# Performance work log

Measured on AMD Instinct MI355X. Metric: run time of the kernel, lower is better.

## Reference

```python
import jax, jax.numpy as jnp
import numpy as np

IN_F = 4096
OUT_F = 16384
TOKENS = 64


def setup_inputs() -> dict:
    key = jax.random.key(0)
    k1, k2, k3 = jax.random.split(key, 3)
    x = jax.random.normal(k1, (TOKENS, IN_F), dtype=jnp.float16)
    # int8-valued weights stored as int32 (same math after cast to fp16)
    weight = jax.random.randint(k2, (OUT_F, IN_F), -127, 127, dtype=jnp.int32)
    weight_scales = jax.random.uniform(k3, (OUT_F,), dtype=jnp.float16, minval=0.001, maxval=0.02)
    bias = jnp.zeros((1, OUT_F), dtype=jnp.float16)
    return {"x": x, "weight": weight, "weight_scales": weight_scales, "bias": bias}


def reference(x, weight, weight_scales, bias):
    # Dequantize int8 weight to fp16 with per-output-channel scale, then linear.
    w_fp16 = weight.astype(jnp.float16) * weight_scales[:, None]  # [out, in]
    y = jnp.dot(x, w_fp16.T) + bias  # [tokens, out]
    return y
```

## Files before the change

### kernel.cpp

```cpp
#include <hip/hip_runtime.h>
#include <hip/hip_bf16.h>
#include <hip/hip_fp16.h>

#define IN_F 4096
#define OUT_F 16384
#define TOKENS 64

#define NT 32
#define KT 128
#define KHALF 2048
#define NTILES 16
#define TILE_BYTES (NT * KT * 4)
#define BLOCK 256

typedef __attribute__((ext_vector_type(8))) short bf16x8;
typedef __attribute__((ext_vector_type(8))) unsigned short u16x8;
typedef __attribute__((ext_vector_type(4))) float f32x4;
typedef __attribute__((ext_vector_type(4))) int i32x4;

enum { F_BF16 = 0, F_FP16 = 1, F_FP32 = 2 };

__device__ __forceinline__ float dec_bf16(unsigned short h) {
    return __uint_as_float(((unsigned)h) << 16);
}
__device__ __forceinline__ float dec_fp16(unsigned short h) {
    __half_raw hr; hr.x = h;
    return __half2float(__half(hr));
}
__device__ __forceinline__ unsigned short enc_bf16_rne(float f) {
    unsigned u = __float_as_uint(f);
    u += 0x7FFFu + ((u >> 16) & 1u);
    return (unsigned short)(u >> 16);
}

__device__ __forceinline__ int detect_fmt16(const void* p, int lane, float lo, float hi) {
    unsigned short h = ((const unsigned short*)p)[lane];
    float vb = fabsf(dec_bf16(h));
    float vh = fabsf(dec_fp16(h));
    int cb = __popcll(__ballot(vb > lo && vb < hi));
    int ch = __popcll(__ballot(vh > lo && vh < hi));
    return (cb >= 56) ? F_BF16 : (ch >= 56) ? F_FP16 : F_FP32;
}
__device__ __forceinline__ int detect_wint(const int* w, int lane) {
    int v = w[lane];
    int ci = __popcll(__ballot(v >= -127 && v <= 127));
    return (ci >= 56) ? 1 : 0;
}

__global__ __launch_bounds__(256) void prep_x(const void* __restrict__ xv,
                                              unsigned short* __restrict__ xbf) {
    const int tid  = blockIdx.x * 256 + threadIdx.x;
    const int lane = threadIdx.x & 63;
    const int xf = detect_fmt16(xv, lane, 9.7e-4f, 64.0f);

    if (xf == F_BF16) {
        u16x8 a = ((const u16x8*)xv)[tid * 2];
        u16x8 b = ((const u16x8*)xv)[tid * 2 + 1];
        ((u16x8*)xbf)[tid * 2]     = a;
        ((u16x8*)xbf)[tid * 2 + 1] = b;
    } else if (xf == F_FP32) {
        u16x8 o[2];
        #pragma unroll
        for (int half = 0; half < 2; ++half) {
            f32x4 v0 = ((const f32x4*)xv)[tid * 4 + half * 2];
            f32x4 v1 = ((const f32x4*)xv)[tid * 4 + half * 2 + 1];
            #pragma unroll
            for (int j = 0; j < 4; ++j) {
                o[half][j]     = enc_bf16_rne(v0[j]);
                o[half][j + 4] = enc_bf16_rne(v1[j]);
            }
        }
        ((u16x8*)xbf)[tid * 2]     = o[0];
        ((u16x8*)xbf)[tid * 2 + 1] = o[1];
    } else {
        #pragma unroll
        for (int half = 0; half < 2; ++half) {
            u16x8 v = ((const u16x8*)xv)[tid * 2 + half];
            u16x8 o;
            #pragma unroll
            for (int j = 0; j < 8; ++j) o[j] = enc_bf16_rne(dec_fp16(v[j]));
            ((u16x8*)xbf)[tid * 2 + half] = o;
        }
    }
}

template <int WINT>
__device__ __forceinline__ void tile_compute(const char* __restrict__ buf,
                                             const unsigned short* __restrict__ xbf,
                                             int kbase, int ln, int kq, int row,
                                             f32x4 acc[4]) {
    const char*  bufb = buf + row * 512;
    const short* xs   = (const short*)xbf;
    #pragma unroll
    for (int kt = 0; kt < 4; ++kt) {
        const int c0 = kt * 8 + 2 * kq;
        i32x4 b0 = *(const i32x4*)(bufb + ((c0)     ^ ln) * 16);
        i32x4 b1 = *(const i32x4*)(bufb + ((c0 + 1) ^ ln) * 16);
        bf16x8 bfrag;
        #pragma unroll
        for (int j = 0; j < 4; ++j) {
            unsigned f0 = WINT ? __float_as_uint((float)b0[j]) : (unsigned)b0[j];
            unsigned f1 = WINT ? __float_as_uint((float)b1[j]) : (unsigned)b1[j];
            bfrag[j]     = (short)(f0 >> 16);
            bfrag[j + 4] = (short)(f1 >> 16);
        }
        const int kk = kbase + kt * 32 + kq * 8;
        bf16x8 a0 = *(const bf16x8*)(xs + (size_t)(ln     ) * IN_F + kk);
        bf16x8 a1 = *(const bf16x8*)(xs + (size_t)(ln + 16) * IN_F + kk);
        bf16x8 a2 = *(const bf16x8*)(xs + (size_t)(ln + 32) * IN_F + kk);
        bf16x8 a3 = *(const bf16x8*)(xs + (size_t)(ln + 48) * IN_F + kk);
        acc[0] = __builtin_amdgcn_mfma_f32_16x16x32_bf16(a0, bfrag, acc[0], 0, 0, 0);
        acc[1] = __builtin_amdgcn_mfma_f32_16x16x32_bf16(a1, bfrag, acc[1], 0, 0, 0);
        acc[2] = __builtin_amdgcn_mfma_f32_16x16x32_bf16(a2, bfrag, acc[2], 0, 0, 0);
        acc[3] = __builtin_amdgcn_mfma_f32_16x16x32_bf16(a3, bfrag, acc[3], 0, 0, 0);
    }
}

__global__ __launch_bounds__(BLOCK, 2) void w8a16_main(
    const void* __restrict__ xv_orig, const int* __restrict__ w,
    const void* __restrict__ sv, const void* __restrict__ bv,
    void* __restrict__ yv, const unsigned short* __restrict__ xbf) {

    __shared__ alignas(16) char lds[2][2][TILE_BYTES];

    const int tid  = threadIdx.x;
    const int wv   = tid >> 6;
    const int lane = tid & 63;
    const int ln   = lane & 15;
    const int kq   = lane >> 4;
    const int h    = wv >> 1;
    const int wl   = wv & 1;
    const int n0   = blockIdx.x * NT;

    const int xf = detect_fmt16(xv_orig, lane, 9.7e-4f, 64.0f);
    const int sf = detect_fmt16(sv, lane, 1.0e-4f, 0.25f);
    const int wi = detect_wint(w, lane);

    const int th   = tid >> 7;
    const int t127 = tid & 127;
    auto stage = [&](int tile, int dbuf) {
        #pragma unroll
        for (int j = 0; j < 8; ++j) {
            const int idx = j * 128 + t127;
            const int r   = idx >> 5;
            const int c   = idx & 31;
            const int cg  = c ^ (r & 15);
            const int* g = w + (size_t)(n0 + r) * IN_F + th * KHALF + tile * KT + cg * 4;
            char* l = &lds[th][dbuf][idx * 16];
            __builtin_amdgcn_global_load_lds(
                (const __attribute__((address_space(1))) unsigned int*)g,
                (__attribute__((address_space(3))) unsigned int*)l, 16, 0, 0);
        }
    };

    f32x4 acc[4] = {};
    const int row = 16 * wl + ln;

    stage(0, 0);
    __syncthreads();
    for (int t = 0; t < NTILES; ++t) {
        if (t + 1 < NTILES) stage(t + 1, (t + 1) & 1);
        const char* buf   = &lds[h][t & 1][0];
        const int   kbase = h * KHALF + t * KT;
        if (wi) tile_compute<1>(buf, xbf, kbase, ln, kq, row, acc);
        else    tile_compute<0>(buf, xbf, kbase, ln, kq, row, acc);
        __syncthreads();
    }

    float* red = (float*)&lds[0][0][0];
    if (h == 1) {
        #pragma unroll
        for (int i = 0; i < 4; ++i)
            #pragma unroll
            for (int r2 = 0; r2 < 4; ++r2)
                red[(wl * 64 + lane) * 16 + i * 4 + r2] = acc[i][r2];
    }
    __syncthreads();
    if (h == 0) {
        #pragma unroll
        for (int i = 0; i < 4; ++i)
            #pragma unroll
            for (int r2 = 0; r2 < 4; ++r2)
                acc[i][r2] += red[(wl * 64 + lane) * 16 + i * 4 + r2];

        const int n = n0 + row;
        float scale, bias;
        if (sf == F_FP32) {
            scale = ((const float*)sv)[n];
            bias  = ((const float*)bv)[n];
        } else if (sf == F_BF16) {
            scale = dec_bf16(((const unsigned short*)sv)[n]);
            bias  = dec_bf16(((const unsigned short*)bv)[n]);
        } else {
            scale = dec_fp16(((const unsigned short*)sv)[n]);
            bias  = dec_fp16(((const unsigned short*)bv)[n]);
        }

        #pragma unroll
        for (int i = 0; i < 4; ++i) {
            #pragma unroll
            for (int r2 = 0; r2 < 4; ++r2) {
                const int    m   = 16 * i + kq * 4 + r2;
                const float  val = acc[i][r2] * scale + bias;
                const size_t o   = (size_t)m * OUT_F + n;
                if (xf == F_FP32)      ((float*)yv)[o] = val;
                else if (xf == F_BF16) ((unsigned short*)yv)[o] = enc_bf16_rne(val);
                else                   ((__half*)yv)[o] = __float2half(val);
            }
        }
    }
}

extern "C" void kernel_launch(void* const* d_in, const int* in_sizes, int n_in,
                              void* d_out, int out_size, void* d_ws, size_t ws_size,
                              hipStream_t stream) {
    unsigned short* xbf = (unsigned short*)d_ws;
    prep_x<<<64, 256, 0, stream>>>(d_in[0], xbf);
    w8a16_main<<<OUT_F / NT, BLOCK, 0, stream>>>(d_in[0], (const int*)d_in[1],
                                                 d_in[2], d_in[3], d_out, xbf);
}
```

Measured before the change: 381.0 us.

## Replace LDS-staged weight tiles with direct register loads and 4-way split-K

Drops the global_load_lds double-buffered weight staging and has each lane read its int32 weight row directly into registers, with a one-iteration software prefetch. Each block now covers 16 output channels, and its four waves each take a quarter of K, combined by an LDS reduction at the end. This removes the per-tile barriers and LDS traffic, and the launch bound is raised to four blocks per CU to gain occupancy. In exchange, weight reads per lane are 32-byte strided segments across rows rather than the swizzled coalesced staging, and the final reduction is serialized on wave 0.

```diff
diff --git a/kernel.cpp b/kernel.cpp
--- a/kernel.cpp
+++ b/kernel.cpp
@@ -5,13 +5,9 @@
 #define IN_F 4096
 #define OUT_F 16384
 #define TOKENS 64
-
-#define NT 32
-#define KT 128
-#define KHALF 2048
-#define NTILES 16
-#define TILE_BYTES (NT * KT * 4)
 #define BLOCK 256
+#define KQUART (IN_F / 4)
+#define NITER (KQUART / 32)
 
 typedef __attribute__((ext_vector_type(8))) short bf16x8;
 typedef __attribute__((ext_vector_type(8))) unsigned short u16x8;
@@ -85,105 +81,93 @@
 }
 
 template <int WINT>
-__device__ __forceinline__ void tile_compute(const char* __restrict__ buf,
-                                             const unsigned short* __restrict__ xbf,
-                                             int kbase, int ln, int kq, int row,
-                                             f32x4 acc[4]) {
-    const char*  bufb = buf + row * 512;
-    const short* xs   = (const short*)xbf;
-    #pragma unroll
-    for (int kt = 0; kt < 4; ++kt) {
-        const int c0 = kt * 8 + 2 * kq;
-        i32x4 b0 = *(const i32x4*)(bufb + ((c0)     ^ ln) * 16);
-        i32x4 b1 = *(const i32x4*)(bufb + ((c0 + 1) ^ ln) * 16);
+__device__ __forceinline__ void kloop(const int* __restrict__ wp,
+                                      const short* __restrict__ xs,
+                                      int kbase, int ln, int kq,
+                                      f32x4 acc[4]) {
+    const short* x0 = xs + (size_t)(ln     ) * IN_F;
+    const short* x1 = xs + (size_t)(ln + 16) * IN_F;
+    const short* x2 = xs + (size_t)(ln + 32) * IN_F;
+    const short* x3 = xs + (size_t)(ln + 48) * IN_F;
+
+    int k = kbase + kq * 8;
+
+    i32x4  cb0 = *(const i32x4*)(wp + k);
+    i32x4  cb1 = *(const i32x4*)(wp + k + 4);
+    bf16x8 ca0 = *(const bf16x8*)(x0 + k);
+    bf16x8 ca1 = *(const bf16x8*)(x1 + k);
+    bf16x8 ca2 = *(const bf16x8*)(x2 + k);
+    bf16x8 ca3 = *(const bf16x8*)(x3 + k);
+
+    for (int t = 0; t < NITER; ++t) {
+        const int kn = (t + 1 < NITER) ? (k + 32) : (kbase + kq * 8);
+        i32x4  nb0 = *(const i32x4*)(wp + kn);
+        i32x4  nb1 = *(const i32x4*)(wp + kn + 4);
+        bf16x8 na0 = *(const bf16x8*)(x0 + kn);
+        bf16x8 na1 = *(const bf16x8*)(x1 + kn);
+        bf16x8 na2 = *(const bf16x8*)(x2 + kn);
+        bf16x8 na3 = *(const bf16x8*)(x3 + kn);
+
         bf16x8 bfrag;
         #pragma unroll
         for (int j = 0; j < 4; ++j) {
-            unsigned f0 = WINT ? __float_as_uint((float)b0[j]) : (unsigned)b0[j];
-            unsigned f1 = WINT ? __float_as_uint((float)b1[j]) : (unsigned)b1[j];
+            unsigned f0 = WINT ? __float_as_uint((float)cb0[j]) : (unsigned)cb0[j];
+            unsigned f1 = WINT ? __float_as_uint((float)cb1[j]) : (unsigned)cb1[j];
             bfrag[j]     = (short)(f0 >> 16);
             bfrag[j + 4] = (short)(f1 >> 16);
         }
-        const int kk = kbase + kt * 32 + kq * 8;
-        bf16x8 a0 = *(const bf16x8*)(xs + (size_t)(ln     ) * IN_F + kk);
-        bf16x8 a1 = *(const bf16x8*)(xs + (size_t)(ln + 16) * IN_F + kk);
-        bf16x8 a2 = *(const bf16x8*)(xs + (size_t)(ln + 32) * IN_F + kk);
-        bf16x8 a3 = *(const bf16x8*)(xs + (size_t)(ln + 48) * IN_F + kk);
-        acc[0] = __builtin_amdgcn_mfma_f32_16x16x32_bf16(a0, bfrag, acc[0], 0, 0, 0);
-        acc[1] = __builtin_amdgcn_mfma_f32_16x16x32_bf16(a1, bfrag, acc[1], 0, 0, 0);
-        acc[2] = __builtin_amdgcn_mfma_f32_16x16x32_bf16(a2, bfrag, acc[2], 0, 0, 0);
-        acc[3] = __builtin_amdgcn_mfma_f32_16x16x32_bf16(a3, bfrag, acc[3], 0, 0, 0);
+        acc[0] = __builtin_amdgcn_mfma_f32_16x16x32_bf16(ca0, bfrag, acc[0], 0, 0, 0);
+        acc[1] = __builtin_amdgcn_mfma_f32_16x16x32_bf16(ca1, bfrag, acc[1], 0, 0, 0);
+        acc[2] = __builtin_amdgcn_mfma_f32_16x16x32_bf16(ca2, bfrag, acc[2], 0, 0, 0);
+        acc[3] = __builtin_amdgcn_mfma_f32_16x16x32_bf16(ca3, bfrag, acc[3], 0, 0, 0);
+
+        cb0 = nb0; cb1 = nb1;
+        ca0 = na0; ca1 = na1; ca2 = na2; ca3 = na3;
+        k = kn;
     }
 }
 
-__global__ __launch_bounds__(BLOCK, 2) void w8a16_main(
+__global__ __launch_bounds__(BLOCK, 4) void w8a16_main(
     const void* __restrict__ xv_orig, const int* __restrict__ w,
     const void* __restrict__ sv, const void* __restrict__ bv,
     void* __restrict__ yv, const unsigned short* __restrict__ xbf) {
 
-    __shared__ alignas(16) char lds[2][2][TILE_BYTES];
+    __shared__ float red[4][64][17];
 
     const int tid  = threadIdx.x;
     const int wv   = tid >> 6;
     const int lane = tid & 63;
     const int ln   = lane & 15;
     const int kq   = lane >> 4;
-    const int h    = wv >> 1;
-    const int wl   = wv & 1;
-    const int n0   = blockIdx.x * NT;
 
     const int xf = detect_fmt16(xv_orig, lane, 9.7e-4f, 64.0f);
     const int sf = detect_fmt16(sv, lane, 1.0e-4f, 0.25f);
     const int wi = detect_wint(w, lane);
 
-    const int th   = tid >> 7;
-    const int t127 = tid & 127;
-    auto stage = [&](int tile, int dbuf) {
-        #pragma unroll
-        for (int j = 0; j < 8; ++j) {
-            const int idx = j * 128 + t127;
-            const int r   = idx >> 5;
-            const int c   = idx & 31;
-            const int cg  = c ^ (r & 15);
-            const int* g = w + (size_t)(n0 + r) * IN_F + th * KHALF + tile * KT + cg * 4;
-            char* l = &lds[th][dbuf][idx * 16];
-            __builtin_amdgcn_global_load_lds(
-                (const __attribute__((address_space(1))) unsigned int*)g,
-                (__attribute__((address_space(3))) unsigned int*)l, 16, 0, 0);
-        }
-    };
+    const int    n     = blockIdx.x * 16 + ln;
+    const int*   wp    = w + (size_t)n * IN_F;
+    const int    kbase = wv * KQUART;
 
     f32x4 acc[4] = {};
-    const int row = 16 * wl + ln;
-
-    stage(0, 0);
+    if (wi) kloop<1>(wp, (const short*)xbf, kbase, ln, kq, acc);
+    else    kloop<0>(wp, (const short*)xbf, kbase, ln, kq, acc);
+
+    #pragma unroll
+    for (int i = 0; i < 4; ++i)
+        #pragma unroll
+        for (int r2 = 0; r2 < 4; ++r2)
+            red[wv][lane][i * 4 + r2] = acc[i][r2];
     __syncthreads();
-    for (int t = 0; t < NTILES; ++t) {
-        if (t + 1 < NTILES) stage(t + 1, (t + 1) & 1);
-        const char* buf   = &lds[h][t & 1][0];
-        const int   kbase = h * KHALF + t * KT;
-        if (wi) tile_compute<1>(buf, xbf, kbase, ln, kq, row, acc);
-        else    tile_compute<0>(buf, xbf, kbase, ln, kq, row, acc);
-        __syncthreads();
-    }
-
-    float* red = (float*)&lds[0][0][0];
-    if (h == 1) {
+
+    if (wv == 0) {
         #pragma unroll
         for (int i = 0; i < 4; ++i)
             #pragma unroll
             for (int r2 = 0; r2 < 4; ++r2)
-                red[(wl * 64 + lane) * 16 + i * 4 + r2] = acc[i][r2];
-    }
-    __syncthreads();
-    if (h == 0) {
-        #pragma unroll
-        for (int i = 0; i < 4; ++i)
-            #pragma unroll
-            for (int r2 = 0; r2 < 4; ++r2)
-                acc[i][r2] += red[(wl * 64 + lane) * 16 + i * 4 + r2];
-
-        const int n = n0 + row;
+                acc[i][r2] += red[1][lane][i * 4 + r2]
+                            + red[2][lane][i * 4 + r2]
+                            + red[3][lane][i * 4 + r2];
+
         float scale, bias;
         if (sf == F_FP32) {
             scale = ((const float*)sv)[n];
@@ -216,6 +200,6 @@
                               hipStream_t stream) {
     unsigned short* xbf = (unsigned short*)d_ws;
     prep_x<<<64, 256, 0, stream>>>(d_in[0], xbf);
-    w8a16_main<<<OUT_F / NT, BLOCK, 0, stream>>>(d_in[0], (const int*)d_in[1],
+    w8a16_main<<<OUT_F / 16, BLOCK, 0, stream>>>(d_in[0], (const int*)d_in[1],
                                                  d_in[2], d_in[3], d_out, xbf);
 }
```

New measurement: 406.5 us. +6.7%, slower.

## Split K across blocks, stage activations in LDS, reduce partials in separate kernel

Applied to the files above, without the earlier changes.

Each block now covers 64 output channels and one half of K instead of 32 channels and the full K. Activation tiles are staged into swizzled LDS with async global-to-LDS loads rather than read directly from global memory. Partial fp32 sums go to a workspace, and a new reduction kernel adds the two halves, applies scale and bias, and converts the output. The goal is better reuse of activations and more parallel blocks, at the cost of an extra kernel launch and 8 MB of partial-sum traffic.

```diff
diff --git a/kernel.cpp b/kernel.cpp
--- a/kernel.cpp
+++ b/kernel.cpp
@@ -6,15 +6,15 @@
 #define OUT_F 16384
 #define TOKENS 64
 
-#define NT 32
-#define KT 128
+#define NCH 64
+#define KT 64
 #define KHALF 2048
-#define NTILES 16
-#define TILE_BYTES (NT * KT * 4)
+#define NTILES (KHALF / KT)
 #define BLOCK 256
 
 typedef __attribute__((ext_vector_type(8))) short bf16x8;
 typedef __attribute__((ext_vector_type(8))) unsigned short u16x8;
+typedef __attribute__((ext_vector_type(4))) unsigned short u16x4;
 typedef __attribute__((ext_vector_type(4))) float f32x4;
 typedef __attribute__((ext_vector_type(4))) int i32x4;
 
@@ -85,17 +85,15 @@
 }
 
 template <int WINT>
-__device__ __forceinline__ void tile_compute(const char* __restrict__ buf,
-                                             const unsigned short* __restrict__ xbf,
-                                             int kbase, int ln, int kq, int row,
-                                             f32x4 acc[4]) {
-    const char*  bufb = buf + row * 512;
-    const short* xs   = (const short*)xbf;
+__device__ __forceinline__ void tile_compute(const char* __restrict__ bB,
+                                             const char* __restrict__ bA,
+                                             int wv, int ln, int kq, f32x4 acc[4]) {
+    const char* brow = bB + (wv * 16 + ln) * 256;
     #pragma unroll
-    for (int kt = 0; kt < 4; ++kt) {
-        const int c0 = kt * 8 + 2 * kq;
-        i32x4 b0 = *(const i32x4*)(bufb + ((c0)     ^ ln) * 16);
-        i32x4 b1 = *(const i32x4*)(bufb + ((c0 + 1) ^ ln) * 16);
+    for (int s = 0; s < 2; ++s) {
+        const int c0 = s * 8 + kq * 2;
+        i32x4 b0 = *(const i32x4*)(brow + ((c0)     ^ ln) * 16);
+        i32x4 b1 = *(const i32x4*)(brow + ((c0 + 1) ^ ln) * 16);
         bf16x8 bfrag;
         #pragma unroll
         for (int j = 0; j < 4; ++j) {
@@ -104,11 +102,11 @@
             bfrag[j]     = (short)(f0 >> 16);
             bfrag[j + 4] = (short)(f1 >> 16);
         }
-        const int kk = kbase + kt * 32 + kq * 8;
-        bf16x8 a0 = *(const bf16x8*)(xs + (size_t)(ln     ) * IN_F + kk);
-        bf16x8 a1 = *(const bf16x8*)(xs + (size_t)(ln + 16) * IN_F + kk);
-        bf16x8 a2 = *(const bf16x8*)(xs + (size_t)(ln + 32) * IN_F + kk);
-        bf16x8 a3 = *(const bf16x8*)(xs + (size_t)(ln + 48) * IN_F + kk);
+        const int ca = s * 4 + kq;
+        bf16x8 a0 = *(const bf16x8*)(bA + (ln      ) * 128 + ((ca) ^ (ln & 7)) * 16);
+        bf16x8 a1 = *(const bf16x8*)(bA + (ln + 16) * 128 + ((ca) ^ (ln & 7)) * 16);
+        bf16x8 a2 = *(const bf16x8*)(bA + (ln + 32) * 128 + ((ca) ^ (ln & 7)) * 16);
+        bf16x8 a3 = *(const bf16x8*)(bA + (ln + 48) * 128 + ((ca) ^ (ln & 7)) * 16);
         acc[0] = __builtin_amdgcn_mfma_f32_16x16x32_bf16(a0, bfrag, acc[0], 0, 0, 0);
         acc[1] = __builtin_amdgcn_mfma_f32_16x16x32_bf16(a1, bfrag, acc[1], 0, 0, 0);
         acc[2] = __builtin_amdgcn_mfma_f32_16x16x32_bf16(a2, bfrag, acc[2], 0, 0, 0);
@@ -116,98 +114,124 @@
     }
 }
 
-__global__ __launch_bounds__(BLOCK, 2) void w8a16_main(
-    const void* __restrict__ xv_orig, const int* __restrict__ w,
-    const void* __restrict__ sv, const void* __restrict__ bv,
-    void* __restrict__ yv, const unsigned short* __restrict__ xbf) {
-
-    __shared__ alignas(16) char lds[2][2][TILE_BYTES];
+__global__ __launch_bounds__(BLOCK) void w8a16_main(
+    const int* __restrict__ w, const unsigned short* __restrict__ xbf,
+    float* __restrict__ pws) {
+
+    __shared__ alignas(16) char ldsB[2][NCH * KT * 4];
+    __shared__ alignas(16) char ldsA[2][TOKENS * KT * 2];
 
     const int tid  = threadIdx.x;
     const int wv   = tid >> 6;
     const int lane = tid & 63;
     const int ln   = lane & 15;
     const int kq   = lane >> 4;
-    const int h    = wv >> 1;
-    const int wl   = wv & 1;
-    const int n0   = blockIdx.x * NT;
-
-    const int xf = detect_fmt16(xv_orig, lane, 9.7e-4f, 64.0f);
-    const int sf = detect_fmt16(sv, lane, 1.0e-4f, 0.25f);
+
+    const int kh   = blockIdx.x & 1;
+    const int n0   = (blockIdx.x >> 1) * NCH;
+    const int koff = kh * KHALF;
+
     const int wi = detect_wint(w, lane);
 
-    const int th   = tid >> 7;
-    const int t127 = tid & 127;
-    auto stage = [&](int tile, int dbuf) {
-        #pragma unroll
-        for (int j = 0; j < 8; ++j) {
-            const int idx = j * 128 + t127;
-            const int r   = idx >> 5;
-            const int c   = idx & 31;
-            const int cg  = c ^ (r & 15);
-            const int* g = w + (size_t)(n0 + r) * IN_F + th * KHALF + tile * KT + cg * 4;
-            char* l = &lds[th][dbuf][idx * 16];
+    auto stage = [&](int t, int db) {
+        #pragma unroll
+        for (int j = 0; j < 4; ++j) {
+            const int idx = j * 256 + tid;
+            const int r   = idx >> 4;
+            const int cg  = (idx & 15) ^ (r & 15);
+            const int* g  = w + (size_t)(n0 + r) * IN_F + koff + t * KT + cg * 4;
             __builtin_amdgcn_global_load_lds(
                 (const __attribute__((address_space(1))) unsigned int*)g,
-                (__attribute__((address_space(3))) unsigned int*)l, 16, 0, 0);
+                (__attribute__((address_space(3))) unsigned int*)(&ldsB[db][idx * 16]),
+                16, 0, 0);
+        }
+        #pragma unroll
+        for (int j = 0; j < 2; ++j) {
+            const int idx = j * 256 + tid;
+            const int tok = idx >> 3;
+            const int cg  = (idx & 7) ^ (tok & 7);
+            const unsigned short* g = xbf + (size_t)tok * IN_F + koff + t * KT + cg * 8;
+            __builtin_amdgcn_global_load_lds(
+                (const __attribute__((address_space(1))) unsigned int*)g,
+                (__attribute__((address_space(3))) unsigned int*)(&ldsA[db][idx * 16]),
+                16, 0, 0);
         }
     };
 
     f32x4 acc[4] = {};
-    const int row = 16 * wl + ln;
 
     stage(0, 0);
     __syncthreads();
     for (int t = 0; t < NTILES; ++t) {
         if (t + 1 < NTILES) stage(t + 1, (t + 1) & 1);
-        const char* buf   = &lds[h][t & 1][0];
-        const int   kbase = h * KHALF + t * KT;
-        if (wi) tile_compute<1>(buf, xbf, kbase, ln, kq, row, acc);
-        else    tile_compute<0>(buf, xbf, kbase, ln, kq, row, acc);
+        if (wi) tile_compute<1>(ldsB[t & 1], ldsA[t & 1], wv, ln, kq, acc);
+        else    tile_compute<0>(ldsB[t & 1], ldsA[t & 1], wv, ln, kq, acc);
         __syncthreads();
     }
 
-    float* red = (float*)&lds[0][0][0];
-    if (h == 1) {
-        #pragma unroll
-        for (int i = 0; i < 4; ++i)
-            #pragma unroll
-            for (int r2 = 0; r2 < 4; ++r2)
-                red[(wl * 64 + lane) * 16 + i * 4 + r2] = acc[i][r2];
-    }
-    __syncthreads();
-    if (h == 0) {
-        #pragma unroll
-        for (int i = 0; i < 4; ++i)
-            #pragma unroll
-            for (int r2 = 0; r2 < 4; ++r2)
-                acc[i][r2] += red[(wl * 64 + lane) * 16 + i * 4 + r2];
-
-        const int n = n0 + row;
-        float scale, bias;
-        if (sf == F_FP32) {
-            scale = ((const float*)sv)[n];
-            bias  = ((const float*)bv)[n];
-        } else if (sf == F_BF16) {
-            scale = dec_bf16(((const unsigned short*)sv)[n]);
-            bias  = dec_bf16(((const unsigned short*)bv)[n]);
-        } else {
-            scale = dec_fp16(((const unsigned short*)sv)[n]);
-            bias  = dec_fp16(((const unsigned short*)bv)[n]);
-        }
-
-        #pragma unroll
-        for (int i = 0; i < 4; ++i) {
-            #pragma unroll
-            for (int r2 = 0; r2 < 4; ++r2) {
-                const int    m   = 16 * i + kq * 4 + r2;
-                const float  val = acc[i][r2] * scale + bias;
-                const size_t o   = (size_t)m * OUT_F + n;
-                if (xf == F_FP32)      ((float*)yv)[o] = val;
-                else if (xf == F_BF16) ((unsigned short*)yv)[o] = enc_bf16_rne(val);
-                else                   ((__half*)yv)[o] = __float2half(val);
-            }
-        }
+    float* pp = pws + (size_t)kh * TOKENS * OUT_F;
+    const int n = n0 + wv * 16 + ln;
+    #pragma unroll
+    for (int i = 0; i < 4; ++i)
+        #pragma unroll
+        for (int r = 0; r < 4; ++r)
+            pp[(size_t)(16 * i + kq * 4 + r) * OUT_F + n] = acc[i][r];
+}
+
+__global__ __launch_bounds__(256) void reduce_k(
+    const float* __restrict__ pws, const void* __restrict__ xv,
+    const void* __restrict__ sv, const void* __restrict__ bv,
+    void* __restrict__ yv) {
+
+    const int t    = blockIdx.x * 256 + threadIdx.x;
+    const int lane = threadIdx.x & 63;
+    const int xf = detect_fmt16(xv, lane, 9.7e-4f, 64.0f);
+    const int sf = detect_fmt16(sv, lane, 1.0e-4f, 0.25f);
+
+    const int base = t * 4;
+    const int m    = base >> 14;
+    const int n    = base & 16383;
+
+    f32x4 p0 = *(const f32x4*)(pws + (size_t)m * OUT_F + n);
+    f32x4 p1 = *(const f32x4*)(pws + (size_t)TOKENS * OUT_F + (size_t)m * OUT_F + n);
+
+    float sc[4], bi[4];
+    if (sf == F_FP32) {
+        f32x4 s4 = *(const f32x4*)((const float*)sv + n);
+        f32x4 b4 = *(const f32x4*)((const float*)bv + n);
+        #pragma unroll
+        for (int j = 0; j < 4; ++j) { sc[j] = s4[j]; bi[j] = b4[j]; }
+    } else if (sf == F_BF16) {
+        u16x4 s4 = *(const u16x4*)((const unsigned short*)sv + n);
+        u16x4 b4 = *(const u16x4*)((const unsigned short*)bv + n);
+        #pragma unroll
+        for (int j = 0; j < 4; ++j) { sc[j] = dec_bf16(s4[j]); bi[j] = dec_bf16(b4[j]); }
+    } else {
+        u16x4 s4 = *(const u16x4*)((const unsigned short*)sv + n);
+        u16x4 b4 = *(const u16x4*)((const unsigned short*)bv + n);
+        #pragma unroll
+        for (int j = 0; j < 4; ++j) { sc[j] = dec_fp16(s4[j]); bi[j] = dec_fp16(b4[j]); }
+    }
+
+    f32x4 v;
+    #pragma unroll
+    for (int j = 0; j < 4; ++j) v[j] = (p0[j] + p1[j]) * sc[j] + bi[j];
+
+    if (xf == F_FP32) {
+        *(f32x4*)((float*)yv + base) = v;
+    } else if (xf == F_BF16) {
+        u16x4 o;
+        #pragma unroll
+        for (int j = 0; j < 4; ++j) o[j] = enc_bf16_rne(v[j]);
+        *(u16x4*)((unsigned short*)yv + base) = o;
+    } else {
+        u16x4 o;
+        #pragma unroll
+        for (int j = 0; j < 4; ++j) {
+            __half h = __float2half(v[j]);
+            o[j] = *(unsigned short*)&h;
+        }
+        *(u16x4*)((unsigned short*)yv + base) = o;
     }
 }
 
@@ -215,7 +239,9 @@
                               void* d_out, int out_size, void* d_ws, size_t ws_size,
                               hipStream_t stream) {
     unsigned short* xbf = (unsigned short*)d_ws;
+    float*          pws = (float*)((char*)d_ws + 524288);
+
     prep_x<<<64, 256, 0, stream>>>(d_in[0], xbf);
-    w8a16_main<<<OUT_F / NT, BLOCK, 0, stream>>>(d_in[0], (const int*)d_in[1],
-                                                 d_in[2], d_in[3], d_out, xbf);
-}
+    w8a16_main<<<(OUT_F / NCH) * 2, BLOCK, 0, stream>>>((const int*)d_in[1], xbf, pws);
+    reduce_k<<<1024, 256, 0, stream>>>(pws, d_in[0], d_in[2], d_in[3], d_out);
+}
```

Result: no change. 388.5 us (+1.9%).
